# Kernel tuning notes

Hardware: AMD Instinct MI355X
Metric: run time of the kernel (lower is better)

Reference implementation:

```python
import jax, jax.numpy as jnp
import numpy as np
import math

B, N, D_MODEL = 2, 2048, 512
H, D_HEAD = 8, 64
D_FF = 2048
LN_EPS = 1e-5


def layer_norm(x, g, b):
    mu = jnp.mean(x, axis=-1, keepdims=True)
    var = jnp.mean(jnp.square(x - mu), axis=-1, keepdims=True)
    return (x - mu) * jax.lax.rsqrt(var + LN_EPS) * g + b


def setup_inputs() -> dict:
    key = jax.random.key(0)
    ks = jax.random.split(key, 12)
    s = lambda fan_in: 1.0 / math.sqrt(fan_in)
    inp = {
        "x": jax.random.normal(ks[0], (B, N, D_MODEL), dtype=jnp.float32),
        "mask": jax.random.randint(ks[1], (B, 1, N, N), 0, 2) > 0,
        # attention_pre: Linear(d_model -> 3*H*D_HEAD)
        "W_qkv": jax.random.uniform(ks[2], (D_MODEL, 3 * H * D_HEAD), minval=-s(D_MODEL), maxval=s(D_MODEL)),
        "b_qkv": jnp.zeros((3 * H * D_HEAD,), jnp.float32),
        # project: Linear(H*D_HEAD -> d_model)
        "W_proj": jax.random.uniform(ks[3], (H * D_HEAD, D_MODEL), minval=-s(H * D_HEAD), maxval=s(H * D_HEAD)),
        "b_proj": jnp.zeros((D_MODEL,), jnp.float32),
        "ln1_g": jnp.ones((D_MODEL,), jnp.float32),
        "ln1_b": jnp.zeros((D_MODEL,), jnp.float32),
        # mlp: fc(512->2048, relu), fc(2048->512, relu)  (activation on every layer)
        "W1": jax.random.uniform(ks[4], (D_MODEL, D_FF), minval=-s(D_MODEL), maxval=s(D_MODEL)),
        "b1": jnp.zeros((D_FF,), jnp.float32),
        "W2": jax.random.uniform(ks[5], (D_FF, D_MODEL), minval=-s(D_FF), maxval=s(D_FF)),
        "b2": jnp.zeros((D_MODEL,), jnp.float32),
        "ln2_g": jnp.ones((D_MODEL,), jnp.float32),
        "ln2_b": jnp.zeros((D_MODEL,), jnp.float32),
    }
    return inp


def reference(x, mask, W_qkv, b_qkv, W_proj, b_proj, ln1_g, ln1_b, W1, b1, W2, b2, ln2_g, ln2_b):
    # --- Attention (manual QKV matmul-softmax-matmul) ---
    qkv = x @ W_qkv + b_qkv                      # [B,N,3*H*Dh]
    q, k, v = jnp.split(qkv, 3, axis=2)          # each [B,N,H*Dh]
    def split_heads(t):
        return t.reshape(B, N, H, D_HEAD).transpose(0, 2, 1, 3)  # [B,H,N,Dh]
    q, k, v = split_heads(q), split_heads(k), split_heads(v)
    score = jnp.einsum('bhnd,bhmd->bhnm', q, k) / math.sqrt(D_HEAD)  # [B,H,N,N]
    score = jnp.where(mask, score, -1e9)
    score = jax.nn.softmax(score, axis=-1)
    attn = jnp.einsum('bhnm,bhmd->bhnd', score, v)   # [B,H,N,Dh]
    attn = attn.transpose(0, 2, 1, 3).reshape(B, N, H * D_HEAD)
    a = attn @ W_proj + b_proj                   # [B,N,D_MODEL]
    # --- residual + LN1 ---
    x = layer_norm(x + a, ln1_g, ln1_b)
    # --- MLP (relu after both layers, dropout p=0 = identity) ---
    m = jax.nn.relu(jax.nn.relu(x @ W1 + b1) @ W2 + b2)
    x = layer_norm(x + m, ln2_g, ln2_b)
    return x
```

## Files before the change

### kernel.cpp

```cpp
#include <hip/hip_runtime.h>
#include <math.h>

constexpr int BATCH  = 2;
constexpr int SEQ    = 2048;
constexpr int DMODEL = 512;
constexpr int NH     = 8;
constexpr int DHEAD  = 64;
constexpr int ROWS   = BATCH * SEQ;
constexpr size_t SZ  = (size_t)ROWS * DMODEL;

typedef __attribute__((ext_vector_type(8))) short bf16x8;
typedef __attribute__((ext_vector_type(4))) float f32x4;

__device__ __forceinline__ ushort f2bf(float f) {
    unsigned u = __float_as_uint(f);
    unsigned r = (u + 0x7FFFu + ((u >> 16) & 1u)) >> 16;
    return (ushort)r;
}

__device__ __forceinline__ unsigned cvtpk_bf16(float lo, float hi) {
    unsigned r;
    asm("v_cvt_pk_bf16_f32 %0, %1, %2" : "=v"(r) : "v"(lo), "v"(hi));
    return r;
}

__device__ __forceinline__ void gload_lds16(const void* g, void* l) {
    __builtin_amdgcn_global_load_lds(
        (const __attribute__((address_space(1))) void*)g,
        (__attribute__((address_space(3))) void*)l, 16, 0, 0);
}

__global__ __launch_bounds__(256) void detect_mask_k(
    const uint4* __restrict__ m, int* __restrict__ flag)
{
    const int i = blockIdx.x * 256 + threadIdx.x;
    const uint4 v = m[i];
    unsigned b0 = 0, b1 = 0;
    #pragma unroll
    for (int c = 0; c < 4; ++c) {
        const unsigned u = (&v.x)[c];
        b0 |= (u > 1u) ? 1u : 0u;
        b1 |= (u != 0u && u != 0x3F800000u) ? 1u : 0u;
    }
    const int lane = threadIdx.x & 63;
    if (__any(b0) && lane == 0) atomicOr(flag, 1);
    if (__any(b1) && lane == 0) atomicOr(flag, 2);
}

__global__ __launch_bounds__(256) void prep_all_k(
    const float* __restrict__ x, ushort* __restrict__ xb,
    const float* __restrict__ Wq, const float* __restrict__ Wp,
    const float* __restrict__ W1w, const float* __restrict__ W2w,
    ushort* __restrict__ WqT, ushort* __restrict__ WpT,
    ushort* __restrict__ W1T, ushort* __restrict__ W2T,
    const void* __restrict__ maskp, const int* __restrict__ flagp,
    unsigned long long* __restrict__ bits)
{
    __shared__ ushort T[64][65];
    const int bid = blockIdx.x;
    const int t = threadIdx.x;

    if (bid < 2048) {
        const size_t i = ((size_t)bid * 256 + t) * 4;
        float4 v = *(const float4*)(x + i);
        ushort4 o;
        o.x = f2bf(v.x); o.y = f2bf(v.y); o.z = f2bf(v.z); o.w = f2bf(v.w);
        *(ushort4*)(xb + i) = o;
        return;
    }
    if (bid >= 2816) {
        const int w = (bid - 2816) * 4 + (t >> 6);
        const int lane = t & 63;
        const size_t idx = ((size_t)w << 6) + lane;
        const int f = *flagp;
        bool mv;
        if (!(f & 1))      mv = ((const int*)maskp)[idx] != 0;
        else if (!(f & 2)) mv = ((const float*)maskp)[idx] != 0.f;
        else               mv = ((const unsigned char*)maskp)[idx] != 0;
        unsigned long long bal = __ballot(mv);
        if (lane == 0) bits[w] = bal;
        return;
    }
    const int wb = bid - 2048;
    const float* W; ushort* Wt; int K, N, tix, tiy;
    if (wb < 192)      { W = Wq;  Wt = WqT; K = 512;  N = 1536; tix = wb % 24;        tiy = wb / 24; }
    else if (wb < 256) { W = Wp;  Wt = WpT; K = 512;  N = 512;  tix = (wb-192) % 8;   tiy = (wb-192) / 8; }
    else if (wb < 512) { W = W1w; Wt = W1T; K = 512;  N = 2048; tix = (wb-256) % 32;  tiy = (wb-256) / 32; }
    else               { W = W2w; Wt = W2T; K = 2048; N = 512;  tix = (wb-512) % 8;   tiy = (wb-512) / 8; }
    const int k0 = tiy * 64, n0 = tix * 64;
    const int r = t >> 4, c4 = (t & 15) * 4;
    #pragma unroll
    for (int it = 0; it < 4; ++it) {
        const int row = it*16 + r;
        float4 v = *(const float4*)&W[(size_t)(k0 + row) * N + n0 + c4];
        T[c4+0][row] = f2bf(v.x);
        T[c4+1][row] = f2bf(v.y);
        T[c4+2][row] = f2bf(v.z);
        T[c4+3][row] = f2bf(v.w);
    }
    __syncthreads();
    #pragma unroll
    for (int it = 0; it < 4; ++it) {
        const int row = it*16 + r;
        ushort4 o;
        o.x = T[row][c4+0]; o.y = T[row][c4+1];
        o.z = T[row][c4+2]; o.w = T[row][c4+3];
        *(ushort4*)&Wt[(size_t)(n0 + row) * K + k0 + c4] = o;
    }
}

template<int EPI, int BM>
__global__ __launch_bounds__(256) void mgemm_k(
    const ushort* __restrict__ A,
    const ushort* __restrict__ Wt,
    const float* __restrict__ bias,
    float* __restrict__ Cf, ushort* __restrict__ Cb,
    ushort* __restrict__ Qo, ushort* __restrict__ Ko, ushort* __restrict__ Vo,
    int M, int N, int K)
{
    constexpr int WM   = BM / 2;
    constexpr int MF   = WM / 16;
    constexpr int APW  = (BM / 8) / 4;

    __shared__ ushort As[BM * 64];
    __shared__ ushort Bs[128 * 64];

    const int tid  = threadIdx.x;
    const int wid  = tid >> 6, lane = tid & 63;
    const int lq   = lane & 15, lg = lane >> 4;
    const int wr   = wid >> 1,  wc = wid & 1;
    const int bm   = blockIdx.y * BM, bn = blockIdx.x * 128;

    const int srow0 = lane >> 3;
    const int sch   = lane & 7;

    f32x4 acc[MF][4] = {};

    for (int k0 = 0; k0 < K; k0 += 64) {
        __syncthreads();
        #pragma unroll
        for (int i = 0; i < APW; ++i) {
            const int seg = wid * APW + i;
            const int row = seg * 8 + srow0;
            const int c16 = sch ^ (row & 7);
            gload_lds16(A + (size_t)(bm + row) * K + k0 + c16 * 8, As + seg * 512);
        }
        #pragma unroll
        for (int i = 0; i < 4; ++i) {
            const int seg = wid * 4 + i;
            const int row = seg * 8 + srow0;
            const int c16 = sch ^ (row & 7);
            gload_lds16(Wt + (size_t)(bn + row) * K + k0 + c16 * 8, Bs + seg * 512);
        }
        __syncthreads();

        #pragma unroll
        for (int ks = 0; ks < 2; ++ks) {
            bf16x8 af[MF], bfr[4];
            #pragma unroll
            for (int m = 0; m < MF; ++m) {
                const int row = wr*WM + m*16 + lq;
                const int c16 = (ks*4 + lg) ^ (row & 7);
                af[m] = *(const bf16x8*)&As[row * 64 + c16 * 8];
            }
            #pragma unroll
            for (int n = 0; n < 4; ++n) {
                const int row = wc*64 + n*16 + lq;
                const int c16 = (ks*4 + lg) ^ (row & 7);
                bfr[n] = *(const bf16x8*)&Bs[row * 64 + c16 * 8];
            }
            #pragma unroll
            for (int m = 0; m < MF; ++m)
                #pragma unroll
                for (int n = 0; n < 4; ++n)
                    acc[m][n] = __builtin_amdgcn_mfma_f32_16x16x32_bf16(
                        af[m], bfr[n], acc[m][n], 0, 0, 0);
        }
    }

    #pragma unroll
    for (int m = 0; m < MF; ++m) {
        const int row0 = bm + wr*WM + m*16 + lg*4;
        #pragma unroll
        for (int n = 0; n < 4; ++n) {
            const int col = bn + wc*64 + n*16 + lq;
            const float bv = bias[col];
            float v[4];
            #pragma unroll
            for (int r = 0; r < 4; ++r) {
                v[r] = acc[m][n][r] + bv;
                if (EPI == 1 || EPI == 2) v[r] = fmaxf(v[r], 0.f);
            }
            if (EPI == 3) {
                const int part = col >> 9, hc = col & 511;
                const int hh = hc >> 6, d0 = hc & 63;
                const int bidx = row0 >> 11, nrow0 = row0 & 2047;
                if (part == 2) {
                    ushort4 pv;
                    pv.x = f2bf(v[0]); pv.y = f2bf(v[1]);
                    pv.z = f2bf(v[2]); pv.w = f2bf(v[3]);
                    *(ushort4*)(Vo + (((size_t)bidx*NH + hh)*DHEAD + d0)*SEQ + nrow0) = pv;
                } else {
                    ushort* dst = (part == 0) ? Qo : Ko;
                    #pragma unroll
                    for (int r = 0; r < 4; ++r)
                        dst[((((size_t)bidx*NH + hh)*SEQ + nrow0 + r) << 6) + d0] = f2bf(v[r]);
                }
            } else {
                #pragma unroll
                for (int r = 0; r < 4; ++r) {
                    const int row = row0 + r;
                    if (EPI == 1) Cb[(size_t)row * N + col] = f2bf(v[r]);
                    else          Cf[(size_t)row * N + col] = v[r];
                }
            }
        }
    }
}

__global__ __launch_bounds__(256, 4) void attn_mfma_k(
    const ushort* __restrict__ Qb, const ushort* __restrict__ Kb,
    const ushort* __restrict__ Vtb, const unsigned long long* __restrict__ mbits,
    float* __restrict__ Opart, float2* __restrict__ MLpart)
{
    __shared__ ushort Klds[2][64 * 64];
    __shared__ ushort Vlds[2][64 * 64];
    __shared__ ushort Plds[4][16 * 64];

    const int tid  = threadIdx.x;
    const int wid  = tid >> 6;
    const int lane = tid & 63;
    const int lq   = lane & 15;
    const int lg   = lane >> 4;

    const int tile = blockIdx.x & 31;
    const int bh   = blockIdx.x >> 5;
    const int b    = bh >> 3;
    const int qw   = tile * 64 + wid * 16;
    const int s    = blockIdx.y;
    const int c0   = s * 16, c1 = c0 + 16;

    const ushort* Qg = Qb + ((size_t)bh * SEQ + qw + lq) * DHEAD;
    const bf16x8 qf0 = *(const bf16x8*)(Qg + lg * 8);
    const bf16x8 qf1 = *(const bf16x8*)(Qg + 32 + lg * 8);

    const int srow0 = lane >> 3;
    const int sch   = lane & 7;
    const int gc8   = (sch ^ srow0) * 8;

    const ushort* kgb  = Kb  + (size_t)bh * SEQ * DHEAD
                             + (size_t)(wid*16 + srow0) * DHEAD + gc8;
    const ushort* vgb0 = Vtb + (size_t)bh * DHEAD * SEQ
                             + (size_t)(wid*16 + srow0) * SEQ + gc8;
    const ushort* vgb1 = vgb0 + 8 * SEQ;

    ushort* kd0 = &Klds[0][(wid*2)*512];
    ushort* kd1 = &Klds[1][(wid*2)*512];
    ushort* vd0 = &Vlds[0][(wid*2)*512];
    ushort* vd1 = &Vlds[1][(wid*2)*512];

    int kro[4][2], vro[4][2], pwo[4], pro[2];
    #pragma unroll
    for (int kt = 0; kt < 4; ++kt) {
        kro[kt][0] = ((kt*16 + lq)*64 + ((lg     ^ (lq&7))*8)) * 2;
        kro[kt][1] = ((kt*16 + lq)*64 + (((4+lg) ^ (lq&7))*8)) * 2;
        pwo[kt]    = (wid*1024 + lq*64 + (((kt*2 + (lg>>1)) ^ (lq&7))*8) + (lg&1)*4) * 2;
    }
    #pragma unroll
    for (int kk = 0; kk < 2; ++kk) {
        pro[kk] = (wid*1024 + lq*64 + (((kk*4+lg) ^ (lq&7))*8)) * 2;
        #pragma unroll
        for (int nt = 0; nt < 4; ++nt)
            vro[nt][kk] = ((nt*16 + lq)*64 + (((kk*4+lg) ^ (lq&7))*8)) * 2;
    }
    const char* kbase0 = (const char*)&Klds[0][0];
    const char* kbase1 = (const char*)&Klds[1][0];
    const char* vbase0 = (const char*)&Vlds[0][0];
    const char* vbase1 = (const char*)&Vlds[1][0];
    char*       pbase  = (char*)&Plds[0][0];

    const unsigned long long* mrow = mbits + ((size_t)b * SEQ + qw + lq) * (SEQ / 64);

    f32x4 o[4] = {};
    float mrun = -1e30f, lrun = 0.f;
    const float k2 = 0.125f * 1.44269504f;

    {
        const ushort* kp0  = kgb  + (size_t)c0 * 4096;
        const ushort* vq0  = vgb0 + c0 * 64;
        const ushort* vq1  = vgb1 + c0 * 64;
        gload_lds16(kp0,       kd0);
        gload_lds16(kp0 + 512, kd0 + 512);
        gload_lds16(vq0, vd0);
        gload_lds16(vq1, vd0 + 512);
    }
    const ushort* kp  = kgb  + (size_t)(c0 + 1) * 4096;
    const ushort* vp0 = vgb0 + (c0 + 1) * 64;
    const ushort* vp1 = vgb1 + (c0 + 1) * 64;
    __syncthreads();

#define ATTN_CHUNK(CC, KD, VD, KBASE, VBASE)                                   \
    {                                                                          \
        if ((CC) + 1 < c1) {                                                   \
            gload_lds16(kp,       (KD));                                       \
            gload_lds16(kp + 512, (KD) + 512);                                 \
            gload_lds16(vp0, (VD));                                            \
            gload_lds16(vp1, (VD) + 512);                                      \
            kp += 4096; vp0 += 64; vp1 += 64;                                  \
        }                                                                      \
        f32x4 st[4];                                                           \
        __builtin_amdgcn_s_setprio(1);                                         \
        _Pragma("unroll")                                                      \
        for (int kt = 0; kt < 4; ++kt) {                                       \
            bf16x8 kf0 = *(const bf16x8*)((KBASE) + kro[kt][0]);               \
            bf16x8 kf1 = *(const bf16x8*)((KBASE) + kro[kt][1]);               \
            f32x4 a = {};                                                      \
            a = __builtin_amdgcn_mfma_f32_16x16x32_bf16(kf0, qf0, a, 0, 0, 0); \
            a = __builtin_amdgcn_mfma_f32_16x16x32_bf16(kf1, qf1, a, 0, 0, 0); \
            st[kt] = a;                                                        \
        }                                                                      \
        __builtin_amdgcn_s_setprio(0);                                         \
        const unsigned long long mws = mrow[CC] >> (lg * 4);                   \
        const unsigned mlo = (unsigned)mws, mhi = (unsigned)(mws >> 32);       \
        float sv[16];                                                          \
        _Pragma("unroll")                                                      \
        for (int kt = 0; kt < 4; ++kt) {                                       \
            const unsigned half = (kt & 2) ? mhi : mlo;                        \
            _Pragma("unroll")                                                  \
            for (int r = 0; r < 4; ++r) {                                      \
                const unsigned bit = (half >> ((kt & 1)*16 + r)) & 1u;         \
                sv[kt*4 + r] = bit ? st[kt][r] * k2 : -1e9f;                   \
            }                                                                  \
        }                                                                      \
        float cmax = fmaxf(                                                    \
            fmaxf(fmaxf(fmaxf(sv[0],sv[1]),fmaxf(sv[2],sv[3])),                \
                  fmaxf(fmaxf(sv[4],sv[5]),fmaxf(sv[6],sv[7]))),               \
            fmaxf(fmaxf(fmaxf(sv[8],sv[9]),fmaxf(sv[10],sv[11])),              \
                  fmaxf(fmaxf(sv[12],sv[13]),fmaxf(sv[14],sv[15]))));          \
        cmax = fmaxf(cmax, __shfl_xor(cmax, 16));                              \
        cmax = fmaxf(cmax, __shfl_xor(cmax, 32));                              \
        float mnew = mrun, scale = 1.0f;                                       \
        if (!__all(cmax <= mrun)) {                                            \
            mnew  = fmaxf(mrun, cmax);                                         \
            scale = exp2f(mrun - mnew);                                        \
            float sc[4];                                                       \
            _Pragma("unroll")                                                  \
            for (int r = 0; r < 4; ++r) sc[r] = __shfl(scale, lg*4 + r);       \
            _Pragma("unroll")                                                  \
            for (int nt = 0; nt < 4; ++nt)                                     \
                _Pragma("unroll")                                              \
                for (int r = 0; r < 4; ++r) o[nt][r] *= sc[r];                 \
        }                                                                      \
        float ls[4];                                                           \
        _Pragma("unroll")                                                      \
        for (int kt = 0; kt < 4; ++kt) {                                       \
            const float p0 = exp2f(sv[kt*4+0] - mnew);                         \
            const float p1 = exp2f(sv[kt*4+1] - mnew);                         \
            const float p2 = exp2f(sv[kt*4+2] - mnew);                         \
            const float p3 = exp2f(sv[kt*4+3] - mnew);                         \
            ls[kt] = (p0 + p1) + (p2 + p3);                                    \
            uint2 pk;                                                          \
            pk.x = cvtpk_bf16(p0, p1);                                         \
            pk.y = cvtpk_bf16(p2, p3);                                         \
            *(uint2*)(pbase + pwo[kt]) = pk;                                   \
        }                                                                      \
        float lsum = (ls[0] + ls[1]) + (ls[2] + ls[3]);                        \
        lsum += __shfl_xor(lsum, 16);                                          \
        lsum += __shfl_xor(lsum, 32);                                          \
        lrun = lrun * scale + lsum;                                            \
        mrun = mnew;                                                           \
        __builtin_amdgcn_s_setprio(1);                                         \
        _Pragma("unroll")                                                      \
        for (int kk = 0; kk < 2; ++kk) {                                       \
            bf16x8 pf = *(const bf16x8*)(pbase + pro[kk]);                     \
            _Pragma("unroll")                                                  \
            for (int nt = 0; nt < 4; ++nt) {                                   \
                bf16x8 vf = *(const bf16x8*)((VBASE) + vro[nt][kk]);           \
                o[nt] = __builtin_amdgcn_mfma_f32_16x16x32_bf16(               \
                    pf, vf, o[nt], 0, 0, 0);                                   \
            }                                                                  \
        }                                                                      \
        __builtin_amdgcn_s_setprio(0);                                         \
        __syncthreads();                                                       \
    }

    for (int c = c0; c < c1; c += 2) {
        ATTN_CHUNK(c,     kd1, vd1, kbase0, vbase0);
        ATTN_CHUNK(c + 1, kd0, vd0, kbase1, vbase1);
    }
#undef ATTN_CHUNK

    #pragma unroll
    for (int nt = 0; nt < 4; ++nt)
        #pragma unroll
        for (int r = 0; r < 4; ++r) {
            const int qrow = qw + lg*4 + r;
            Opart[(((size_t)s*16 + bh)*SEQ + qrow)*64 + nt*16 + lq] = o[nt][r];
        }
    if (lg == 0) {
        float2 ml; ml.x = mrun; ml.y = lrun;
        MLpart[((size_t)s*16 + bh)*SEQ + qw + lq] = ml;
    }
}

__global__ __launch_bounds__(256) void attn_combine_k(
    const float* __restrict__ Op, const float2* __restrict__ ML,
    ushort* __restrict__ attnb)
{
    const int row  = blockIdx.x * 4 + (threadIdx.x >> 6);
    const int lane = threadIdx.x & 63;
    const int bh = row >> 11, q = row & 2047;
    const int b = bh >> 3, h = bh & 7;
    const float2 ml0 = ML[row];
    const float2 ml1 = ML[16*SEQ + row];
    const float m  = fmaxf(ml0.x, ml1.x);
    const float a0 = exp2f(ml0.x - m), a1 = exp2f(ml1.x - m);
    const float l  = ml0.y*a0 + ml1.y*a1;
    const float o0 = Op[(size_t)row*64 + lane];
    const float o1 = Op[((size_t)16*SEQ + row)*64 + lane];
    const float o  = (o0*a0 + o1*a1) / l;
    attnb[((size_t)(b*SEQ + q))*DMODEL + h*DHEAD + lane] = f2bf(o);
}

__global__ __launch_bounds__(256) void add_ln_k(
    const float* __restrict__ X, const float* __restrict__ Aa,
    const float* __restrict__ gg, const float* __restrict__ bb,
    float* __restrict__ out, ushort* __restrict__ outb)
{
    const int r = blockIdx.x;
    const int t = threadIdx.x;
    const float2 x2 = ((const float2*)(X  + (size_t)r * DMODEL))[t];
    const float2 a2 = ((const float2*)(Aa + (size_t)r * DMODEL))[t];
    const float v0 = x2.x + a2.x, v1 = x2.y + a2.y;
    float s  = v0 + v1;
    float ss = v0*v0 + v1*v1;
    #pragma unroll
    for (int off = 32; off > 0; off >>= 1) {
        s  += __shfl_down(s,  off);
        ss += __shfl_down(ss, off);
    }
    __shared__ float ps[4], pss[4];
    const int wid = t >> 6;
    if ((t & 63) == 0) { ps[wid] = s; pss[wid] = ss; }
    __syncthreads();
    const float tot  = ps[0] + ps[1] + ps[2] + ps[3];
    const float tots = pss[0] + pss[1] + pss[2] + pss[3];
    const float mean = tot * (1.0f / DMODEL);
    const float var  = tots * (1.0f / DMODEL) - mean * mean;
    const float rstd = rsqrtf(var + 1e-5f);
    const float2 g2 = ((const float2*)gg)[t];
    const float2 b2 = ((const float2*)bb)[t];
    float2 r2;
    r2.x = (v0 - mean) * rstd * g2.x + b2.x;
    r2.y = (v1 - mean) * rstd * g2.y + b2.y;
    ((float2*)(out + (size_t)r * DMODEL))[t] = r2;
    if (outb) {
        ushort2 ob; ob.x = f2bf(r2.x); ob.y = f2bf(r2.y);
        *(ushort2*)(outb + (size_t)r * DMODEL + t*2) = ob;
    }
}

extern "C" void kernel_launch(void* const* d_in, const int* in_sizes, int n_in,
                              void* d_out, int out_size, void* d_ws, size_t ws_size,
                              hipStream_t stream)
{
    const float* x      = (const float*)d_in[0];
    const void*  mask   = d_in[1];
    const float* W_qkv  = (const float*)d_in[2];
    const float* b_qkv  = (const float*)d_in[3];
    const float* W_proj = (const float*)d_in[4];
    const float* b_proj = (const float*)d_in[5];
    const float* ln1_g  = (const float*)d_in[6];
    const float* ln1_b  = (const float*)d_in[7];
    const float* W1     = (const float*)d_in[8];
    const float* b1     = (const float*)d_in[9];
    const float* W2     = (const float*)d_in[10];
    const float* b2     = (const float*)d_in[11];
    const float* ln2_g  = (const float*)d_in[12];
    const float* ln2_b  = (const float*)d_in[13];

    float* ws = (float*)d_ws;
    ushort* xb    = (ushort*)ws;
    ushort* Qb    = (ushort*)(ws + SZ/2);
    ushort* Kb    = (ushort*)(ws + SZ);
    ushort* Vtb   = (ushort*)(ws + SZ + SZ/2);
    ushort* attnb = (ushort*)(ws + 2*SZ);
    float*  Opart = ws + 2*SZ + SZ/2;
    float2* MLp   = (float2*)(ws + 4*SZ + SZ/2);
    float*  ap    = ws + 2*SZ + SZ/2;
    float*  mbuf  = ws + 2*SZ;
    float*  x1    = ws + 3*SZ + SZ/2;
    ushort* x1b   = (ushort*)(ws + 4*SZ + SZ/2);
    ushort* hb    = (ushort*)ws;
    ushort* WqkvT = (ushort*)(ws + 5*SZ);
    ushort* WprojT= (ushort*)(ws + 5*SZ + 393216);
    ushort* W1T   = (ushort*)(ws + 5*SZ + 524288);
    ushort* W2T   = (ushort*)(ws + 5*SZ + 1048576);
    unsigned long long* bits = (unsigned long long*)(ws + 5*SZ + 1572864);
    int*    flag  = (int*)(ws + 5*SZ + 1572864 + 262144);

    float* out = (float*)d_out;

    hipMemsetAsync(flag, 0, 4, stream);
    detect_mask_k<<<64, 256, 0, stream>>>((const uint4*)mask, flag);
    prep_all_k<<<2816 + 32768, 256, 0, stream>>>(
        x, xb, W_qkv, W_proj, W1, W2, WqkvT, WprojT, W1T, W2T,
        mask, flag, bits);

    mgemm_k<3,128><<<dim3(12, 32), 256, 0, stream>>>(xb, WqkvT, b_qkv,
        nullptr, nullptr, Qb, Kb, Vtb, ROWS, 3*DMODEL, DMODEL);
    attn_mfma_k<<<dim3(BATCH*NH*(SEQ/64), 2), 256, 0, stream>>>(
        Qb, Kb, Vtb, bits, Opart, MLp);
    attn_combine_k<<<BATCH*NH*SEQ/4, 256, 0, stream>>>(Opart, MLp, attnb);
    mgemm_k<0,64><<<dim3(4, 64), 256, 0, stream>>>(attnb, WprojT, b_proj,
        ap, nullptr, nullptr, nullptr, nullptr, ROWS, DMODEL, DMODEL);
    add_ln_k<<<ROWS, 256, 0, stream>>>(x, ap, ln1_g, ln1_b, x1, x1b);
    mgemm_k<1,128><<<dim3(16, 32), 256, 0, stream>>>(x1b, W1T, b1,
        nullptr, hb, nullptr, nullptr, nullptr, ROWS, 2048, DMODEL);
    mgemm_k<2,64><<<dim3(4, 64), 256, 0, stream>>>(hb, W2T, b2,
        mbuf, nullptr, nullptr, nullptr, nullptr, ROWS, DMODEL, 2048);
    add_ln_k<<<ROWS, 256, 0, stream>>>(x1, mbuf, ln2_g, ln2_b, out, nullptr);
}
```

Baseline: 172.0 us.

## Shrink GEMM tiles, split attention keys four ways, store partials in bf16

The GEMM kernel gains a BN template parameter, and all four GEMMs launch with smaller tiles (64x128 or 64x64), doubling the block count so more of the machine's compute units are busy. Flash attention now splits the key dimension into four chunks instead of two. Partial outputs are stored as bf16 to halve their write and read traffic, and the combine kernel merges the four partials. The trade-offs are less data reuse per tile, more combine work, and lower precision in the partial outputs.

Result: faster. 161.1 us (-6.3%).

```diff
diff --git a/kernel.cpp b/kernel.cpp
--- a/kernel.cpp
+++ b/kernel.cpp
@@ -8,6 +8,7 @@
 constexpr int DHEAD  = 64;
 constexpr int ROWS   = BATCH * SEQ;
 constexpr size_t SZ  = (size_t)ROWS * DMODEL;
+constexpr int NSPLIT = 4;
 
 typedef __attribute__((ext_vector_type(8))) short bf16x8;
 typedef __attribute__((ext_vector_type(4))) float f32x4;
@@ -16,6 +17,9 @@
     unsigned u = __float_as_uint(f);
     unsigned r = (u + 0x7FFFu + ((u >> 16) & 1u)) >> 16;
     return (ushort)r;
+}
+__device__ __forceinline__ float bf2f(ushort u) {
+    return __uint_as_float((unsigned)u << 16);
 }
 
 __device__ __forceinline__ unsigned cvtpk_bf16(float lo, float hi) {
@@ -109,7 +113,7 @@
     }
 }
 
-template<int EPI, int BM>
+template<int EPI, int BM, int BN>
 __global__ __launch_bounds__(256) void mgemm_k(
     const ushort* __restrict__ A,
     const ushort* __restrict__ Wt,
@@ -118,23 +122,24 @@
     ushort* __restrict__ Qo, ushort* __restrict__ Ko, ushort* __restrict__ Vo,
     int M, int N, int K)
 {
-    constexpr int WM   = BM / 2;
-    constexpr int MF   = WM / 16;
-    constexpr int APW  = (BM / 8) / 4;
+    constexpr int WM  = BM / 2, WN = BN / 2;
+    constexpr int MF  = WM / 16, NF = WN / 16;
+    constexpr int APW = BM / 32;
+    constexpr int BPW = BN / 32;
 
     __shared__ ushort As[BM * 64];
-    __shared__ ushort Bs[128 * 64];
+    __shared__ ushort Bs[BN * 64];
 
     const int tid  = threadIdx.x;
     const int wid  = tid >> 6, lane = tid & 63;
     const int lq   = lane & 15, lg = lane >> 4;
     const int wr   = wid >> 1,  wc = wid & 1;
-    const int bm   = blockIdx.y * BM, bn = blockIdx.x * 128;
+    const int bm   = blockIdx.y * BM, bn = blockIdx.x * BN;
 
     const int srow0 = lane >> 3;
     const int sch   = lane & 7;
 
-    f32x4 acc[MF][4] = {};
+    f32x4 acc[MF][NF] = {};
 
     for (int k0 = 0; k0 < K; k0 += 64) {
         __syncthreads();
@@ -146,8 +151,8 @@
             gload_lds16(A + (size_t)(bm + row) * K + k0 + c16 * 8, As + seg * 512);
         }
         #pragma unroll
-        for (int i = 0; i < 4; ++i) {
-            const int seg = wid * 4 + i;
+        for (int i = 0; i < BPW; ++i) {
+            const int seg = wid * BPW + i;
             const int row = seg * 8 + srow0;
             const int c16 = sch ^ (row & 7);
             gload_lds16(Wt + (size_t)(bn + row) * K + k0 + c16 * 8, Bs + seg * 512);
@@ -156,7 +161,7 @@
 
         #pragma unroll
         for (int ks = 0; ks < 2; ++ks) {
-            bf16x8 af[MF], bfr[4];
+            bf16x8 af[MF], bfr[NF];
             #pragma unroll
             for (int m = 0; m < MF; ++m) {
                 const int row = wr*WM + m*16 + lq;
@@ -164,15 +169,15 @@
                 af[m] = *(const bf16x8*)&As[row * 64 + c16 * 8];
             }
             #pragma unroll
-            for (int n = 0; n < 4; ++n) {
-                const int row = wc*64 + n*16 + lq;
+            for (int n = 0; n < NF; ++n) {
+                const int row = wc*WN + n*16 + lq;
                 const int c16 = (ks*4 + lg) ^ (row & 7);
                 bfr[n] = *(const bf16x8*)&Bs[row * 64 + c16 * 8];
             }
             #pragma unroll
             for (int m = 0; m < MF; ++m)
                 #pragma unroll
-                for (int n = 0; n < 4; ++n)
+                for (int n = 0; n < NF; ++n)
                     acc[m][n] = __builtin_amdgcn_mfma_f32_16x16x32_bf16(
                         af[m], bfr[n], acc[m][n], 0, 0, 0);
         }
@@ -182,8 +187,8 @@
     for (int m = 0; m < MF; ++m) {
         const int row0 = bm + wr*WM + m*16 + lg*4;
         #pragma unroll
-        for (int n = 0; n < 4; ++n) {
-            const int col = bn + wc*64 + n*16 + lq;
+        for (int n = 0; n < NF; ++n) {
+            const int col = bn + wc*WN + n*16 + lq;
             const float bv = bias[col];
             float v[4];
             #pragma unroll
@@ -221,7 +226,7 @@
 __global__ __launch_bounds__(256, 4) void attn_mfma_k(
     const ushort* __restrict__ Qb, const ushort* __restrict__ Kb,
     const ushort* __restrict__ Vtb, const unsigned long long* __restrict__ mbits,
-    float* __restrict__ Opart, float2* __restrict__ MLpart)
+    ushort* __restrict__ Opart, float2* __restrict__ MLpart)
 {
     __shared__ ushort Klds[2][64 * 64];
     __shared__ ushort Vlds[2][64 * 64];
@@ -238,7 +243,7 @@
     const int b    = bh >> 3;
     const int qw   = tile * 64 + wid * 16;
     const int s    = blockIdx.y;
-    const int c0   = s * 16, c1 = c0 + 16;
+    const int c0   = s * 8, c1 = c0 + 8;
 
     const ushort* Qg = Qb + ((size_t)bh * SEQ + qw + lq) * DHEAD;
     const bf16x8 qf0 = *(const bf16x8*)(Qg + lg * 8);
@@ -395,7 +400,7 @@
         #pragma unroll
         for (int r = 0; r < 4; ++r) {
             const int qrow = qw + lg*4 + r;
-            Opart[(((size_t)s*16 + bh)*SEQ + qrow)*64 + nt*16 + lq] = o[nt][r];
+            Opart[(((size_t)s*16 + bh)*SEQ + qrow)*64 + nt*16 + lq] = f2bf(o[nt][r]);
         }
     if (lg == 0) {
         float2 ml; ml.x = mrun; ml.y = lrun;
@@ -404,22 +409,28 @@
 }
 
 __global__ __launch_bounds__(256) void attn_combine_k(
-    const float* __restrict__ Op, const float2* __restrict__ ML,
+    const ushort* __restrict__ Op, const float2* __restrict__ ML,
     ushort* __restrict__ attnb)
 {
     const int row  = blockIdx.x * 4 + (threadIdx.x >> 6);
     const int lane = threadIdx.x & 63;
     const int bh = row >> 11, q = row & 2047;
     const int b = bh >> 3, h = bh & 7;
-    const float2 ml0 = ML[row];
-    const float2 ml1 = ML[16*SEQ + row];
-    const float m  = fmaxf(ml0.x, ml1.x);
-    const float a0 = exp2f(ml0.x - m), a1 = exp2f(ml1.x - m);
-    const float l  = ml0.y*a0 + ml1.y*a1;
-    const float o0 = Op[(size_t)row*64 + lane];
-    const float o1 = Op[((size_t)16*SEQ + row)*64 + lane];
-    const float o  = (o0*a0 + o1*a1) / l;
-    attnb[((size_t)(b*SEQ + q))*DMODEL + h*DHEAD + lane] = f2bf(o);
+    float2 ml[NSPLIT];
+    float m = -1e30f;
+    #pragma unroll
+    for (int s = 0; s < NSPLIT; ++s) {
+        ml[s] = ML[(size_t)s*16*SEQ + row];
+        m = fmaxf(m, ml[s].x);
+    }
+    float l = 0.f, o = 0.f;
+    #pragma unroll
+    for (int s = 0; s < NSPLIT; ++s) {
+        const float a = exp2f(ml[s].x - m);
+        l += ml[s].y * a;
+        o += bf2f(Op[((size_t)s*16*SEQ + row)*64 + lane]) * a;
+    }
+    attnb[((size_t)(b*SEQ + q))*DMODEL + h*DHEAD + lane] = f2bf(o / l);
 }
 
 __global__ __launch_bounds__(256) void add_ln_k(
@@ -485,7 +496,7 @@
     ushort* Kb    = (ushort*)(ws + SZ);
     ushort* Vtb   = (ushort*)(ws + SZ + SZ/2);
     ushort* attnb = (ushort*)(ws + 2*SZ);
-    float*  Opart = ws + 2*SZ + SZ/2;
+    ushort* Opart = (ushort*)(ws + 2*SZ + SZ/2);
     float2* MLp   = (float2*)(ws + 4*SZ + SZ/2);
     float*  ap    = ws + 2*SZ + SZ/2;
     float*  mbuf  = ws + 2*SZ;
@@ -507,17 +518,17 @@
         x, xb, W_qkv, W_proj, W1, W2, WqkvT, WprojT, W1T, W2T,
         mask, flag, bits);
 
-    mgemm_k<3,128><<<dim3(12, 32), 256, 0, stream>>>(xb, WqkvT, b_qkv,
+    mgemm_k<3,64,128><<<dim3(12, 64), 256, 0, stream>>>(xb, WqkvT, b_qkv,
         nullptr, nullptr, Qb, Kb, Vtb, ROWS, 3*DMODEL, DMODEL);
-    attn_mfma_k<<<dim3(BATCH*NH*(SEQ/64), 2), 256, 0, stream>>>(
+    attn_mfma_k<<<dim3(BATCH*NH*(SEQ/64), NSPLIT), 256, 0, stream>>>(
         Qb, Kb, Vtb, bits, Opart, MLp);
     attn_combine_k<<<BATCH*NH*SEQ/4, 256, 0, stream>>>(Opart, MLp, attnb);
-    mgemm_k<0,64><<<dim3(4, 64), 256, 0, stream>>>(attnb, WprojT, b_proj,
+    mgemm_k<0,64,64><<<dim3(8, 64), 256, 0, stream>>>(attnb, WprojT, b_proj,
         ap, nullptr, nullptr, nullptr, nullptr, ROWS, DMODEL, DMODEL);
     add_ln_k<<<ROWS, 256, 0, stream>>>(x, ap, ln1_g, ln1_b, x1, x1b);
-    mgemm_k<1,128><<<dim3(16, 32), 256, 0, stream>>>(x1b, W1T, b1,
+    mgemm_k<1,64,128><<<dim3(16, 64), 256, 0, stream>>>(x1b, W1T, b1,
         nullptr, hb, nullptr, nullptr, nullptr, ROWS, 2048, DMODEL);
-    mgemm_k<2,64><<<dim3(4, 64), 256, 0, stream>>>(hb, W2T, b2,
+    mgemm_k<2,64,64><<<dim3(8, 64), 256, 0, stream>>>(hb, W2T, b2,
         mbuf, nullptr, nullptr, nullptr, nullptr, ROWS, DMODEL, 2048);
     add_ln_k<<<ROWS, 256, 0, stream>>>(x1, mbuf, ln2_g, ln2_b, out, nullptr);
 }
```
